# Performance work log

Hardware: AMD Instinct MI355X
Metric: run time of the kernel (lower is better)

## Reference

```python
import jax, jax.numpy as jnp
import numpy as np


def setup_inputs() -> dict:
    key = jax.random.key(0)
    kx, ke = jax.random.split(key)
    N, T, D, M = 64, 400, 1024, 256
    x = jax.random.normal(kx, (N, T, D), dtype=jnp.float32)
    embedding = jax.random.normal(ke, (M, D), dtype=jnp.float32)
    return {"x": x, "embedding": embedding}


def reference(x, embedding):
    # x: (N, T, D); embedding (codebook): (M, D)
    M, D = embedding.shape
    # L2_distance: normalize codebook rows, distances to detached x
    emb_norm = embedding / (jnp.linalg.norm(embedding, axis=1, keepdims=True) + 1e-4)
    x_flat = jax.lax.stop_gradient(x).reshape(-1, D)  # (N*T, D)
    distances = (jnp.sum(emb_norm ** 2, axis=1)[None, :]
                 + jnp.sum(x_flat ** 2, axis=1, keepdims=True)
                 - 2.0 * (x_flat @ emb_norm.T))  # (N*T, M)
    indices = jnp.argmin(distances, axis=-1)  # (N*T,)
    encodings = jax.nn.one_hot(indices, M, dtype=jnp.float32)  # (N*T, M)
    quantized = embedding[indices].reshape(x.shape)  # gather from UNnormalized codebook

    # commitment loss (both sides detached in original -> constant)
    commitment_loss = jnp.mean(
        (jax.lax.stop_gradient(x) - jax.lax.stop_gradient(quantized)) ** 2)

    # straight-through + average with quantized
    quantized_st = x + jax.lax.stop_gradient(quantized - x)
    quantized_ = (quantized_st + quantized) / 2.0

    avg_probs = jnp.mean(encodings, axis=0)  # (M,)
    perplexity = jnp.exp(-jnp.sum(avg_probs * jnp.log(avg_probs + 1e-10)))
    return quantized_, commitment_loss, perplexity
```

## Files before the change

kernel.cpp:

```cpp
#include <hip/hip_runtime.h>
#include <cstdint>
#include <cstddef>


typedef __attribute__((ext_vector_type(8))) short short8;
typedef __attribute__((ext_vector_type(4))) float f32x4;

namespace {
constexpr int kNT = 25600;
constexpr int kD  = 1024;
constexpr int kM  = 256;
constexpr size_t kQElems = (size_t)kNT * kD;

constexpr int WS_IMG_H = 0;
constexpr int WS_IMG_L = 131072;
constexpr int WS_E2N   = 262144;
constexpr int WS_SCL   = WS_E2N + kM;
constexpr int WS_E2R   = WS_SCL + kM;
constexpr int WS_COM   = WS_E2R + kM;
constexpr int WS_HIST  = WS_COM + 4;
constexpr int WS_ZERO_BYTES = (WS_HIST + kM - WS_COM) * 4;
}

typedef __attribute__((address_space(3))) unsigned int        lds_u32;
typedef const __attribute__((address_space(1))) unsigned int  glb_u32;
typedef const __attribute__((address_space(3))) char          lds_chc;

__device__ __forceinline__ void gl2lds16(const void* g, void* l) {
  __builtin_amdgcn_global_load_lds((glb_u32*)g, (lds_u32*)l, 16, 0, 0);
}

template <int OFF>
__device__ __forceinline__ short8 ldsr(lds_chc* p) {
  short8 r;
  asm volatile("ds_read_b128 %0, %1 offset:%c2" : "=v"(r) : "v"(p), "i"(OFF));
  return r;
}

__global__ __launch_bounds__(256) void vq_normalize(const float* __restrict__ emb,
                                                    float* __restrict__ ws) {
  const int m = blockIdx.x;
  const int t = threadIdx.x;
  const float4 v = reinterpret_cast<const float4*>(emb + (size_t)m * kD)[t];
  float s = v.x * v.x + v.y * v.y + v.z * v.z + v.w * v.w;
#pragma unroll
  for (int mask = 32; mask >= 1; mask >>= 1) s += __shfl_xor(s, mask);
  __shared__ float red[4];
  if ((t & 63) == 0) red[t >> 6] = s;
  __syncthreads();
  const float tot = red[0] + red[1] + red[2] + red[3];
  const float sc  = sqrtf(tot) + 1e-4f;
  const float inv = 1.0f / sc;
  const float4 nv = make_float4(v.x * inv, v.y * inv, v.z * inv, v.w * inv);

  float s2 = nv.x * nv.x + nv.y * nv.y + nv.z * nv.z + nv.w * nv.w;
#pragma unroll
  for (int mask = 32; mask >= 1; mask >>= 1) s2 += __shfl_xor(s2, mask);
  __syncthreads();
  if ((t & 63) == 0) red[t >> 6] = s2;
  __syncthreads();
  if (t == 0) {
    ws[WS_E2N + m] = red[0] + red[1] + red[2] + red[3];
    ws[WS_SCL + m] = sc;
    ws[WS_E2R + m] = tot;
  }

  unsigned short* imgh = (unsigned short*)(ws + WS_IMG_H);
  unsigned short* imgl = (unsigned short*)(ws + WS_IMG_L);
  const int c  = t >> 3;
  const int g  = (t >> 1) & 3;
  const int sq = g ^ ((m >> 1) & 3);
  const int base = c * 8192 + m * 32 + sq * 8 + 4 * (t & 1);
  ushort4 hq, lq;
#pragma unroll
  for (int j = 0; j < 4; ++j) {
    const float fv = (&nv.x)[j];
    const unsigned int b = __float_as_uint(fv);
    const unsigned short hi = (unsigned short)(b >> 16);
    const float lof = fv - __uint_as_float(b & 0xFFFF0000u);
    const unsigned short lo = (unsigned short)(__float_as_uint(lof) >> 16);
    (&hq.x)[j] = hi; (&lq.x)[j] = lo;
  }
  *(ushort4*)(imgh + base) = hq;
  *(ushort4*)(imgl + base) = lq;
}


#define RD8(BSEL, G, H0, H1, H2, H3, L0, L1, L2, L3)                           \
  H0 = ldsr<(BSEL) * 32768 + ((G) * 4 + 0) * 1024>(lbase);                     \
  H1 = ldsr<(BSEL) * 32768 + ((G) * 4 + 1) * 1024>(lbase);                     \
  H2 = ldsr<(BSEL) * 32768 + ((G) * 4 + 2) * 1024>(lbase);                     \
  H3 = ldsr<(BSEL) * 32768 + ((G) * 4 + 3) * 1024>(lbase);                     \
  L0 = ldsr<(BSEL) * 32768 + 16384 + ((G) * 4 + 0) * 1024>(lbase);             \
  L1 = ldsr<(BSEL) * 32768 + 16384 + ((G) * 4 + 1) * 1024>(lbase);             \
  L2 = ldsr<(BSEL) * 32768 + 16384 + ((G) * 4 + 2) * 1024>(lbase);             \
  L3 = ldsr<(BSEL) * 32768 + 16384 + ((G) * 4 + 3) * 1024>(lbase);

#define MM12(G, H0, H1, H2, H3, L0, L1, L2, L3)                                              \
  acc[(G) * 4 + 0] = __builtin_amdgcn_mfma_f32_16x16x32_bf16(ah, H0, acc[(G) * 4 + 0], 0, 0, 0); \
  acc[(G) * 4 + 1] = __builtin_amdgcn_mfma_f32_16x16x32_bf16(ah, H1, acc[(G) * 4 + 1], 0, 0, 0); \
  acc[(G) * 4 + 2] = __builtin_amdgcn_mfma_f32_16x16x32_bf16(ah, H2, acc[(G) * 4 + 2], 0, 0, 0); \
  acc[(G) * 4 + 3] = __builtin_amdgcn_mfma_f32_16x16x32_bf16(ah, H3, acc[(G) * 4 + 3], 0, 0, 0); \
  acc[(G) * 4 + 0] = __builtin_amdgcn_mfma_f32_16x16x32_bf16(ah, L0, acc[(G) * 4 + 0], 0, 0, 0); \
  acc[(G) * 4 + 1] = __builtin_amdgcn_mfma_f32_16x16x32_bf16(ah, L1, acc[(G) * 4 + 1], 0, 0, 0); \
  acc[(G) * 4 + 2] = __builtin_amdgcn_mfma_f32_16x16x32_bf16(ah, L2, acc[(G) * 4 + 2], 0, 0, 0); \
  acc[(G) * 4 + 3] = __builtin_amdgcn_mfma_f32_16x16x32_bf16(ah, L3, acc[(G) * 4 + 3], 0, 0, 0); \
  acc[(G) * 4 + 0] = __builtin_amdgcn_mfma_f32_16x16x32_bf16(al, H0, acc[(G) * 4 + 0], 0, 0, 0); \
  acc[(G) * 4 + 1] = __builtin_amdgcn_mfma_f32_16x16x32_bf16(al, H1, acc[(G) * 4 + 1], 0, 0, 0); \
  acc[(G) * 4 + 2] = __builtin_amdgcn_mfma_f32_16x16x32_bf16(al, H2, acc[(G) * 4 + 2], 0, 0, 0); \
  acc[(G) * 4 + 3] = __builtin_amdgcn_mfma_f32_16x16x32_bf16(al, H3, acc[(G) * 4 + 3], 0, 0, 0);

#define VQ_ITER(KC, BSEL, XC0, XC1, XN0, XN1)                                  \
  {                                                                            \
    const int kcn_ = ((KC) < 31) ? (KC) + 1 : 31;                              \
    const float* xp_ = xrow + kcn_ * 32;                                       \
    XN0 = *(const float4*)xp_;                                                 \
    XN1 = *(const float4*)(xp_ + 4);                                           \
    {                                                                          \
      const unsigned short* sg_ = simg + ((size_t)kcn_ << 13) + soff;          \
      char* dg_ = &buf[(BSEL) ^ 1][0] + ldst;                                  \
      _Pragma("unroll")                                                        \
      for (int it_ = 0; it_ < 8; ++it_)                                        \
        gl2lds16(sg_ + it_ * 512, dg_ + it_ * 1024);                           \
    }                                                                          \
    asm volatile("s_waitcnt vmcnt(10)" ::: "memory");                          \
    __builtin_amdgcn_s_barrier();                                              \
    asm volatile("" ::: "memory");                                             \
    short8 ha0_, ha1_, ha2_, ha3_, la0_, la1_, la2_, la3_;                     \
    short8 hb0_, hb1_, hb2_, hb3_, lb0_, lb1_, lb2_, lb3_;                     \
    RD8((BSEL), 0, ha0_, ha1_, ha2_, ha3_, la0_, la1_, la2_, la3_)             \
    RD8((BSEL), 1, hb0_, hb1_, hb2_, hb3_, lb0_, lb1_, lb2_, lb3_)             \
    short8 ah, al;                                                             \
    {                                                                          \
      union { short8 v; unsigned short u[8]; } H_, L_;                         \
      const float fx_[8] = {XC0.x, XC0.y, XC0.z, XC0.w,                        \
                            XC1.x, XC1.y, XC1.z, XC1.w};                       \
      _Pragma("unroll")                                                        \
      for (int jj_ = 0; jj_ < 8; ++jj_) {                                      \
        const float fv_ = fx_[jj_];                                            \
        const unsigned int b_ = __float_as_uint(fv_);                          \
        H_.u[jj_] = (unsigned short)(b_ >> 16);                                \
        const float lo_ = fv_ - __uint_as_float(b_ & 0xFFFF0000u);             \
        L_.u[jj_] = (unsigned short)(__float_as_uint(lo_) >> 16);              \
        x2 += fv_ * fv_;                                                       \
      }                                                                        \
      ah = H_.v; al = L_.v;                                                    \
    }                                                                          \
    asm volatile("s_waitcnt lgkmcnt(8)" ::: "memory");                         \
    __builtin_amdgcn_sched_barrier(0);                                         \
    MM12(0, ha0_, ha1_, ha2_, ha3_, la0_, la1_, la2_, la3_)                    \
    RD8((BSEL), 2, ha0_, ha1_, ha2_, ha3_, la0_, la1_, la2_, la3_)             \
    asm volatile("s_waitcnt lgkmcnt(8)" ::: "memory");                         \
    __builtin_amdgcn_sched_barrier(0);                                         \
    MM12(1, hb0_, hb1_, hb2_, hb3_, lb0_, lb1_, lb2_, lb3_)                    \
    RD8((BSEL), 3, hb0_, hb1_, hb2_, hb3_, lb0_, lb1_, lb2_, lb3_)             \
    asm volatile("s_waitcnt lgkmcnt(8)" ::: "memory");                         \
    __builtin_amdgcn_sched_barrier(0);                                         \
    MM12(2, ha0_, ha1_, ha2_, ha3_, la0_, la1_, la2_, la3_)                    \
    asm volatile("s_waitcnt lgkmcnt(0)" ::: "memory");                         \
    __builtin_amdgcn_sched_barrier(0);                                         \
    MM12(3, hb0_, hb1_, hb2_, hb3_, lb0_, lb1_, lb2_, lb3_)                    \
    asm volatile("" ::: "memory");                                             \
    __builtin_amdgcn_s_barrier();                                              \
    asm volatile("" ::: "memory");                                             \
  }

__global__ __launch_bounds__(256, 2) void vq_main(const float* __restrict__ x,
                                                  const float* __restrict__ emb,
                                                  const float* __restrict__ wsc,
                                                  float* __restrict__ out,
                                                  float* __restrict__ commit_sum,
                                                  int* __restrict__ hist) {
  __shared__ char buf[2][32768];

  const int t   = threadIdx.x;
  const int l   = t & 63;
  const int w   = t >> 6;
  const int r0  = blockIdx.x * 64 + w * 16;
  const int nlo = l & 15;
  const int q   = l >> 4;
  const int sq  = q ^ ((l >> 1) & 3);

  const unsigned short* imgH = (const unsigned short*)(wsc + WS_IMG_H);
  const unsigned short* imgL = (const unsigned short*)(wsc + WS_IMG_L);
  const unsigned short* simg = (w & 2) ? imgL : imgH;
  const int soff = (w & 1) * 4096 + l * 8;
  const int ldst = w * 8192;

  const float* xrow = x + (size_t)(r0 + nlo) * kD + q * 8;
  lds_chc* lbase = (lds_chc*)&buf[0][0] + nlo * 64 + sq * 16;

  f32x4 acc[16];
#pragma unroll
  for (int i = 0; i < 16; ++i) acc[i] = (f32x4)0.0f;
  float x2 = 0.0f;

  float4 xa0, xa1, xb0, xb1;
  xa0 = *(const float4*)xrow;
  xa1 = *(const float4*)(xrow + 4);
  {
    const unsigned short* sg = simg + soff;
    char* dg = &buf[0][0] + ldst;
#pragma unroll
    for (int it = 0; it < 8; ++it) gl2lds16(sg + it * 512, dg + it * 1024);
  }

#pragma unroll 1
  for (int kk = 0; kk < 32; kk += 2) {
    VQ_ITER(kk,     0, xa0, xa1, xb0, xb1)
    VQ_ITER(kk + 1, 1, xb0, xb1, xa0, xa1)
  }

  x2 += __shfl_xor(x2, 16);
  x2 += __shfl_xor(x2, 32);

  float bv[4] = {3.0e38f, 3.0e38f, 3.0e38f, 3.0e38f};
  int   bj[4] = {0, 0, 0, 0};
#pragma unroll
  for (int ct = 0; ct < 16; ++ct) {
    const int j = ct * 16 + nlo;
    const float e = wsc[WS_E2N + j];
#pragma unroll
    for (int rg = 0; rg < 4; ++rg) {
      const float v = e - 2.0f * acc[ct][rg];
      if (v < bv[rg] || (v == bv[rg] && j < bj[rg])) { bv[rg] = v; bj[rg] = j; }
    }
  }
#pragma unroll
  for (int mk = 1; mk <= 8; mk <<= 1) {
#pragma unroll
    for (int rg = 0; rg < 4; ++rg) {
      const float ov = __shfl_xor(bv[rg], mk);
      const int   oj = __shfl_xor(bj[rg], mk);
      if (ov < bv[rg] || (ov == bv[rg] && oj < bj[rg])) { bv[rg] = ov; bj[rg] = oj; }
    }
  }

  float clq = 0.0f;
#pragma unroll
  for (int rg = 0; rg < 4; ++rg) {
    const int j = bj[rg];
    const float xr2 = __shfl(x2, (q << 2) | rg);
    clq += xr2 + wsc[WS_E2R + j] - (wsc[WS_E2N + j] - bv[rg]) * wsc[WS_SCL + j];
  }
  if (nlo == 0) {
#pragma unroll
    for (int rg = 0; rg < 4; ++rg) atomicAdd(&hist[bj[rg]], 1);
  }
  float cs = (nlo == 0) ? clq : 0.0f;
  cs += __shfl_xor(cs, 16);
  cs += __shfl_xor(cs, 32);
  if (l == 0) atomicAdd(commit_sum, cs);

  const float4* emb4 = (const float4*)emb;
  float4* out4 = (float4*)out;
#pragma unroll
  for (int r = 0; r < 16; ++r) {
    const int j = __shfl(bj[r & 3], (r >> 2) << 4);
    const float4* s = emb4 + (size_t)j * (kD / 4);
    float4* d = out4 + (size_t)(r0 + r) * (kD / 4);
#pragma unroll
    for (int c = 0; c < 4; ++c) d[c * 64 + l] = s[c * 64 + l];
  }
}

__global__ __launch_bounds__(256) void vq_final(const int* __restrict__ hist,
                                                const float* __restrict__ commit_sum,
                                                float* __restrict__ out) {
  const int t = threadIdx.x;
  const float p = (float)hist[t] * (1.0f / (float)kNT);
  float s = p * logf(p + 1e-10f);
#pragma unroll
  for (int mask = 32; mask >= 1; mask >>= 1) s += __shfl_xor(s, mask);
  __shared__ float red[4];
  if ((t & 63) == 0) red[t >> 6] = s;
  __syncthreads();
  if (t == 0) {
    const float ent = red[0] + red[1] + red[2] + red[3];
    out[kQElems]     = commit_sum[0] * (1.0f / (float)kQElems);
    out[kQElems + 1] = expf(-ent);
  }
}

extern "C" void kernel_launch(void* const* d_in, const int* in_sizes, int n_in,
                              void* d_out, int out_size, void* d_ws, size_t ws_size,
                              hipStream_t stream) {
  (void)in_sizes; (void)n_in; (void)out_size; (void)ws_size;
  const float* x   = (const float*)d_in[0];
  const float* emb = (const float*)d_in[1];
  float* out = (float*)d_out;
  float* ws  = (float*)d_ws;

  hipMemsetAsync((char*)d_ws + (size_t)WS_COM * 4, 0, WS_ZERO_BYTES, stream);
  hipLaunchKernelGGL(vq_normalize, dim3(kM), dim3(256), 0, stream, emb, ws);
  hipLaunchKernelGGL(vq_main, dim3(kNT / 64), dim3(256), 0, stream,
                     x, emb, ws, out, ws + WS_COM, (int*)(ws + WS_HIST));
  hipLaunchKernelGGL(vq_final, dim3(1), dim3(256), 0, stream,
                     (const int*)(ws + WS_HIST), ws + WS_COM, out);
}
```

Baseline: 252.6 us.

## Repartition VQ GEMM so each wave owns a codebook slice with shared x tile

Restructures the main distance GEMM. Each wave now keeps its own 64-code slice of the bf16 hi/lo codebook in LDS, and the 64 rows of x are converted once and written into a shared LDS tile that all waves read as the A operand. Previously each wave held 16 rows and all 256 codes. The argmin is then done per wave and merged across waves through shared memory. The change also restages the pipeline (x loads two steps ahead, MFMA priority via setprio) and cuts LDS per block to 48KB. The aim is to reduce redundant codebook LDS reads and improve MFMA/DMA overlap, at the cost of a cross-wave reduction and extra barriers.

```diff
diff --git a/kernel.cpp b/kernel.cpp
--- a/kernel.cpp
+++ b/kernel.cpp
@@ -36,6 +36,15 @@
   asm volatile("ds_read_b128 %0, %1 offset:%c2" : "=v"(r) : "v"(p), "i"(OFF));
   return r;
 }
+template <int OFF>
+__device__ __forceinline__ void ldsw(lds_chc* p, short8 v) {
+  asm volatile("ds_write_b128 %0, %1 offset:%c2" :: "v"(p), "v"(v), "i"(OFF) : "memory");
+}
+__device__ __forceinline__ f32x4 gld4(const float* p) {
+  f32x4 r;
+  asm volatile("global_load_dwordx4 %0, %1, off" : "=v"(r) : "v"(p));
+  return r;
+}
 
 __global__ __launch_bounds__(256) void vq_normalize(const float* __restrict__ emb,
                                                     float* __restrict__ ws) {
@@ -86,83 +95,94 @@
 }
 
 
-#define RD8(BSEL, G, H0, H1, H2, H3, L0, L1, L2, L3)                           \
-  H0 = ldsr<(BSEL) * 32768 + ((G) * 4 + 0) * 1024>(lbase);                     \
-  H1 = ldsr<(BSEL) * 32768 + ((G) * 4 + 1) * 1024>(lbase);                     \
-  H2 = ldsr<(BSEL) * 32768 + ((G) * 4 + 2) * 1024>(lbase);                     \
-  H3 = ldsr<(BSEL) * 32768 + ((G) * 4 + 3) * 1024>(lbase);                     \
-  L0 = ldsr<(BSEL) * 32768 + 16384 + ((G) * 4 + 0) * 1024>(lbase);             \
-  L1 = ldsr<(BSEL) * 32768 + 16384 + ((G) * 4 + 1) * 1024>(lbase);             \
-  L2 = ldsr<(BSEL) * 32768 + 16384 + ((G) * 4 + 2) * 1024>(lbase);             \
-  L3 = ldsr<(BSEL) * 32768 + 16384 + ((G) * 4 + 3) * 1024>(lbase);
-
-#define MM12(G, H0, H1, H2, H3, L0, L1, L2, L3)                                              \
-  acc[(G) * 4 + 0] = __builtin_amdgcn_mfma_f32_16x16x32_bf16(ah, H0, acc[(G) * 4 + 0], 0, 0, 0); \
-  acc[(G) * 4 + 1] = __builtin_amdgcn_mfma_f32_16x16x32_bf16(ah, H1, acc[(G) * 4 + 1], 0, 0, 0); \
-  acc[(G) * 4 + 2] = __builtin_amdgcn_mfma_f32_16x16x32_bf16(ah, H2, acc[(G) * 4 + 2], 0, 0, 0); \
-  acc[(G) * 4 + 3] = __builtin_amdgcn_mfma_f32_16x16x32_bf16(ah, H3, acc[(G) * 4 + 3], 0, 0, 0); \
-  acc[(G) * 4 + 0] = __builtin_amdgcn_mfma_f32_16x16x32_bf16(ah, L0, acc[(G) * 4 + 0], 0, 0, 0); \
-  acc[(G) * 4 + 1] = __builtin_amdgcn_mfma_f32_16x16x32_bf16(ah, L1, acc[(G) * 4 + 1], 0, 0, 0); \
-  acc[(G) * 4 + 2] = __builtin_amdgcn_mfma_f32_16x16x32_bf16(ah, L2, acc[(G) * 4 + 2], 0, 0, 0); \
-  acc[(G) * 4 + 3] = __builtin_amdgcn_mfma_f32_16x16x32_bf16(ah, L3, acc[(G) * 4 + 3], 0, 0, 0); \
-  acc[(G) * 4 + 0] = __builtin_amdgcn_mfma_f32_16x16x32_bf16(al, H0, acc[(G) * 4 + 0], 0, 0, 0); \
-  acc[(G) * 4 + 1] = __builtin_amdgcn_mfma_f32_16x16x32_bf16(al, H1, acc[(G) * 4 + 1], 0, 0, 0); \
-  acc[(G) * 4 + 2] = __builtin_amdgcn_mfma_f32_16x16x32_bf16(al, H2, acc[(G) * 4 + 2], 0, 0, 0); \
-  acc[(G) * 4 + 3] = __builtin_amdgcn_mfma_f32_16x16x32_bf16(al, H3, acc[(G) * 4 + 3], 0, 0, 0);
-
-#define VQ_ITER(KC, BSEL, XC0, XC1, XN0, XN1)                                  \
+#define DMASTAGE(KCN)                                                          \
   {                                                                            \
-    const int kcn_ = ((KC) < 31) ? (KC) + 1 : 31;                              \
-    const float* xp_ = xrow + kcn_ * 32;                                       \
-    XN0 = *(const float4*)xp_;                                                 \
-    XN1 = *(const float4*)(xp_ + 4);                                           \
+    const unsigned short* gh_ = imgH + ((size_t)(KCN) << 13) + (w << 11) + (l << 3); \
+    const unsigned short* gl_ = imgL + ((size_t)(KCN) << 13) + (w << 11) + (l << 3); \
+    gl2lds16(gh_,        BslU);                                                \
+    gl2lds16(gh_ +  512, BslU + 1024);                                         \
+    gl2lds16(gh_ + 1024, BslU + 2048);                                         \
+    gl2lds16(gh_ + 1536, BslU + 3072);                                         \
+    gl2lds16(gl_,        BslU + 4096);                                         \
+    gl2lds16(gl_ +  512, BslU + 5120);                                         \
+    gl2lds16(gl_ + 1024, BslU + 6144);                                         \
+    gl2lds16(gl_ + 1536, BslU + 7168);                                         \
+  }
+
+#define CONV8(F0, F1, AH, AL)                                                  \
+  {                                                                            \
+    union { short8 v; unsigned short u[8]; } H_, L_;                           \
+    _Pragma("unroll")                                                          \
+    for (int jj_ = 0; jj_ < 8; ++jj_) {                                        \
+      const float fv_ = (jj_ < 4) ? (F0)[jj_] : (F1)[jj_ - 4];                 \
+      const unsigned int b_ = __float_as_uint(fv_);                            \
+      H_.u[jj_] = (unsigned short)(b_ >> 16);                                  \
+      const float lo_ = fv_ - __uint_as_float(b_ & 0xFFFF0000u);               \
+      L_.u[jj_] = (unsigned short)(__float_as_uint(lo_) >> 16);                \
+      x2 += fv_ * fv_;                                                         \
+    }                                                                          \
+    AH = H_.v; AL = L_.v;                                                      \
+  }
+
+#define MMQ(AR, B0, B1, B2, B3, RT)                                                        \
+  acc[RT][0] = __builtin_amdgcn_mfma_f32_16x16x32_bf16(AR, B0, acc[RT][0], 0, 0, 0);       \
+  acc[RT][1] = __builtin_amdgcn_mfma_f32_16x16x32_bf16(AR, B1, acc[RT][1], 0, 0, 0);       \
+  acc[RT][2] = __builtin_amdgcn_mfma_f32_16x16x32_bf16(AR, B2, acc[RT][2], 0, 0, 0);       \
+  acc[RT][3] = __builtin_amdgcn_mfma_f32_16x16x32_bf16(AR, B3, acc[RT][3], 0, 0, 0);
+#define MMPASS(A0, A1, A2, A3, B0, B1, B2, B3)                                 \
+  MMQ(A0, B0, B1, B2, B3, 0) MMQ(A1, B0, B1, B2, B3, 1)                        \
+  MMQ(A2, B0, B1, B2, B3, 2) MMQ(A3, B0, B1, B2, B3, 3)
+
+#define VQ_ITER5(KC, XB, XC0, XC1, XN0, XN1)                                   \
+  {                                                                            \
+    asm volatile("s_waitcnt vmcnt(2)" ::: "memory");          \
+    __builtin_amdgcn_sched_barrier(0);                                         \
+    short8 a0h, a1h, a2h, a3h, a0l, a1l, a2l, a3l;                             \
+    short8 b0h, b1h, b2h, b3h, b0l, b1l, b2l, b3l;                             \
+    a0h = ldsr<32768 + (XB) * 8192 + 0 * 1024>(pA);                            \
+    a1h = ldsr<32768 + (XB) * 8192 + 1 * 1024>(pA);                            \
+    a2h = ldsr<32768 + (XB) * 8192 + 2 * 1024>(pA);                            \
+    a3h = ldsr<32768 + (XB) * 8192 + 3 * 1024>(pA);                            \
+    a0l = ldsr<32768 + (XB) * 8192 + 4096 + 0 * 1024>(pA);                     \
+    a1l = ldsr<32768 + (XB) * 8192 + 4096 + 1 * 1024>(pA);                     \
+    a2l = ldsr<32768 + (XB) * 8192 + 4096 + 2 * 1024>(pA);                     \
+    a3l = ldsr<32768 + (XB) * 8192 + 4096 + 3 * 1024>(pA);                     \
+    b0h = ldsr<0 * 1024>(pB);                                                  \
+    b1h = ldsr<1 * 1024>(pB);                                                  \
+    b2h = ldsr<2 * 1024>(pB);                                                  \
+    b3h = ldsr<3 * 1024>(pB);                                                  \
+    b0l = ldsr<4096 + 0 * 1024>(pB);                                           \
+    b1l = ldsr<4096 + 1 * 1024>(pB);                                           \
+    b2l = ldsr<4096 + 2 * 1024>(pB);                                           \
+    b3l = ldsr<4096 + 3 * 1024>(pB);                                           \
+    asm volatile("s_waitcnt lgkmcnt(0)" ::: "memory");      \
+    __builtin_amdgcn_sched_barrier(0);                                         \
+    {                      \
+      const int kcn_ = ((KC) + 1 < 32) ? (KC) + 1 : 31;                        \
+      DMASTAGE(kcn_)                                                           \
+    }                                                                          \
     {                                                                          \
-      const unsigned short* sg_ = simg + ((size_t)kcn_ << 13) + soff;          \
-      char* dg_ = &buf[(BSEL) ^ 1][0] + ldst;                                  \
-      _Pragma("unroll")                                                        \
-      for (int it_ = 0; it_ < 8; ++it_)                                        \
-        gl2lds16(sg_ + it_ * 512, dg_ + it_ * 1024);                           \
+      const int kc2_ = ((KC) + 2 < 32) ? (KC) + 2 : 31;                        \
+      XN0 = gld4(xrow + kc2_ * 32);                                            \
+      XN1 = gld4(xrow + kc2_ * 32 + 4);                                        \
     }                                                                          \
-    asm volatile("s_waitcnt vmcnt(10)" ::: "memory");                          \
+    __builtin_amdgcn_s_setprio(1);                                             \
+    MMPASS(a0h, a1h, a2h, a3h, b0h, b1h, b2h, b3h)                  \
+    MMPASS(a0h, a1h, a2h, a3h, b0l, b1l, b2l, b3l)                  \
+    __builtin_amdgcn_s_setprio(0);                                             \
+    asm volatile("s_waitcnt vmcnt(10)" ::: "memory");       \
+    __builtin_amdgcn_sched_barrier(0);                                         \
+    if ((KC) < 31) {                                                           \
+      short8 cah, cal;                                                         \
+      CONV8(XC0, XC1, cah, cal)                                                \
+      ldsw<32768 + ((XB) ^ 1) * 8192 + 0>(pW, cah);                            \
+      ldsw<32768 + ((XB) ^ 1) * 8192 + 4096>(pW, cal);                         \
+    }                                                                          \
+    __builtin_amdgcn_s_setprio(1);                                             \
+    MMPASS(a0l, a1l, a2l, a3l, b0h, b1h, b2h, b3h)                  \
+    __builtin_amdgcn_s_setprio(0);                                             \
+    asm volatile("s_waitcnt lgkmcnt(0)" ::: "memory");      \
     __builtin_amdgcn_s_barrier();                                              \
-    asm volatile("" ::: "memory");                                             \
-    short8 ha0_, ha1_, ha2_, ha3_, la0_, la1_, la2_, la3_;                     \
-    short8 hb0_, hb1_, hb2_, hb3_, lb0_, lb1_, lb2_, lb3_;                     \
-    RD8((BSEL), 0, ha0_, ha1_, ha2_, ha3_, la0_, la1_, la2_, la3_)             \
-    RD8((BSEL), 1, hb0_, hb1_, hb2_, hb3_, lb0_, lb1_, lb2_, lb3_)             \
-    short8 ah, al;                                                             \
-    {                                                                          \
-      union { short8 v; unsigned short u[8]; } H_, L_;                         \
-      const float fx_[8] = {XC0.x, XC0.y, XC0.z, XC0.w,                        \
-                            XC1.x, XC1.y, XC1.z, XC1.w};                       \
-      _Pragma("unroll")                                                        \
-      for (int jj_ = 0; jj_ < 8; ++jj_) {                                      \
-        const float fv_ = fx_[jj_];                                            \
-        const unsigned int b_ = __float_as_uint(fv_);                          \
-        H_.u[jj_] = (unsigned short)(b_ >> 16);                                \
-        const float lo_ = fv_ - __uint_as_float(b_ & 0xFFFF0000u);             \
-        L_.u[jj_] = (unsigned short)(__float_as_uint(lo_) >> 16);              \
-        x2 += fv_ * fv_;                                                       \
-      }                                                                        \
-      ah = H_.v; al = L_.v;                                                    \
-    }                                                                          \
-    asm volatile("s_waitcnt lgkmcnt(8)" ::: "memory");                         \
-    __builtin_amdgcn_sched_barrier(0);                                         \
-    MM12(0, ha0_, ha1_, ha2_, ha3_, la0_, la1_, la2_, la3_)                    \
-    RD8((BSEL), 2, ha0_, ha1_, ha2_, ha3_, la0_, la1_, la2_, la3_)             \
-    asm volatile("s_waitcnt lgkmcnt(8)" ::: "memory");                         \
-    __builtin_amdgcn_sched_barrier(0);                                         \
-    MM12(1, hb0_, hb1_, hb2_, hb3_, lb0_, lb1_, lb2_, lb3_)                    \
-    RD8((BSEL), 3, hb0_, hb1_, hb2_, hb3_, lb0_, lb1_, lb2_, lb3_)             \
-    asm volatile("s_waitcnt lgkmcnt(8)" ::: "memory");                         \
-    __builtin_amdgcn_sched_barrier(0);                                         \
-    MM12(2, ha0_, ha1_, ha2_, ha3_, la0_, la1_, la2_, la3_)                    \
-    asm volatile("s_waitcnt lgkmcnt(0)" ::: "memory");                         \
-    __builtin_amdgcn_sched_barrier(0);                                         \
-    MM12(3, hb0_, hb1_, hb2_, hb3_, lb0_, lb1_, lb2_, lb3_)                    \
-    asm volatile("" ::: "memory");                                             \
-    __builtin_amdgcn_s_barrier();                                              \
-    asm volatile("" ::: "memory");                                             \
   }
 
 __global__ __launch_bounds__(256, 2) void vq_main(const float* __restrict__ x,
@@ -171,94 +191,138 @@
                                                   float* __restrict__ out,
                                                   float* __restrict__ commit_sum,
                                                   int* __restrict__ hist) {
-  __shared__ char buf[2][32768];
+  __shared__ char pool[49152];
+  __shared__ float x2s[64];
+  __shared__ float bvp[4][64];
+  __shared__ int   bjp[4][64];
+  __shared__ int   idx_s[64];
 
   const int t   = threadIdx.x;
   const int l   = t & 63;
   const int w   = t >> 6;
-  const int r0  = blockIdx.x * 64 + w * 16;
   const int nlo = l & 15;
-  const int q   = l >> 4;
-  const int sq  = q ^ ((l >> 1) & 3);
+  const int kq  = l >> 4;
+  const int blk0 = blockIdx.x * 64;
 
   const unsigned short* imgH = (const unsigned short*)(wsc + WS_IMG_H);
   const unsigned short* imgL = (const unsigned short*)(wsc + WS_IMG_L);
-  const unsigned short* simg = (w & 2) ? imgL : imgH;
-  const int soff = (w & 1) * 4096 + l * 8;
-  const int ldst = w * 8192;
-
-  const float* xrow = x + (size_t)(r0 + nlo) * kD + q * 8;
-  lds_chc* lbase = (lds_chc*)&buf[0][0] + nlo * 64 + sq * 16;
-
-  f32x4 acc[16];
-#pragma unroll
-  for (int i = 0; i < 16; ++i) acc[i] = (f32x4)0.0f;
+  char* BslU = pool + w * 8192;
+
+  const float* xrow = x + (size_t)(blk0 + w * 16 + nlo) * kD + kq * 8;
+
+  const int sqz = kq ^ ((nlo >> 1) & 3);
+  lds_chc* base = (lds_chc*)pool;
+  lds_chc* pA = base + nlo * 64 + sqz * 16;
+  lds_chc* pB = base + w * 8192 + nlo * 64 + sqz * 16;
+  lds_chc* pW = pA + w * 1024;
+
+  f32x4 acc[4][4];
+#pragma unroll
+  for (int i = 0; i < 4; ++i)
+#pragma unroll
+    for (int j = 0; j < 4; ++j) acc[i][j] = (f32x4)0.0f;
   float x2 = 0.0f;
 
-  float4 xa0, xa1, xb0, xb1;
-  xa0 = *(const float4*)xrow;
-  xa1 = *(const float4*)(xrow + 4);
+  f32x4 xa0 = gld4(xrow);
+  f32x4 xa1 = gld4(xrow + 4);
+  DMASTAGE(0)
+  f32x4 xb0 = gld4(xrow + 32);
+  f32x4 xb1 = gld4(xrow + 36);
+  asm volatile("s_waitcnt vmcnt(10)" ::: "memory");
+  __builtin_amdgcn_sched_barrier(0);
   {
-    const unsigned short* sg = simg + soff;
-    char* dg = &buf[0][0] + ldst;
-#pragma unroll
-    for (int it = 0; it < 8; ++it) gl2lds16(sg + it * 512, dg + it * 1024);
-  }
+    short8 cah, cal;
+    CONV8(xa0, xa1, cah, cal)
+    ldsw<32768 + 0>(pW, cah);
+    ldsw<32768 + 4096>(pW, cal);
+  }
+  asm volatile("s_waitcnt lgkmcnt(0)" ::: "memory");
+  __builtin_amdgcn_s_barrier();
 
 #pragma unroll 1
   for (int kk = 0; kk < 32; kk += 2) {
-    VQ_ITER(kk,     0, xa0, xa1, xb0, xb1)
-    VQ_ITER(kk + 1, 1, xb0, xb1, xa0, xa1)
-  }
+    VQ_ITER5(kk,     0, xb0, xb1, xa0, xa1)
+    VQ_ITER5(kk + 1, 1, xa0, xa1, xb0, xb1)
+  }
+
+  asm volatile("s_waitcnt vmcnt(0)"
+               :: "v"(xa0), "v"(xa1), "v"(xb0), "v"(xb1) : "memory");
 
   x2 += __shfl_xor(x2, 16);
   x2 += __shfl_xor(x2, 32);
-
-  float bv[4] = {3.0e38f, 3.0e38f, 3.0e38f, 3.0e38f};
-  int   bj[4] = {0, 0, 0, 0};
-#pragma unroll
-  for (int ct = 0; ct < 16; ++ct) {
-    const int j = ct * 16 + nlo;
-    const float e = wsc[WS_E2N + j];
-#pragma unroll
-    for (int rg = 0; rg < 4; ++rg) {
-      const float v = e - 2.0f * acc[ct][rg];
-      if (v < bv[rg] || (v == bv[rg] && j < bj[rg])) { bv[rg] = v; bj[rg] = j; }
+  if (l < 16) x2s[w * 16 + l] = x2;
+
+  float eN[4];
+#pragma unroll
+  for (int ct = 0; ct < 4; ++ct) eN[ct] = wsc[WS_E2N + w * 64 + ct * 16 + nlo];
+
+  float bv[4][4]; int bj[4][4];
+#pragma unroll
+  for (int rt = 0; rt < 4; ++rt)
+#pragma unroll
+    for (int rg = 0; rg < 4; ++rg) { bv[rt][rg] = 3.0e38f; bj[rt][rg] = 0; }
+#pragma unroll
+  for (int ct = 0; ct < 4; ++ct) {
+    const int j = w * 64 + ct * 16 + nlo;
+#pragma unroll
+    for (int rt = 0; rt < 4; ++rt)
+#pragma unroll
+      for (int rg = 0; rg < 4; ++rg) {
+        const float v = eN[ct] - 2.0f * acc[rt][ct][rg];
+        if (v < bv[rt][rg] || (v == bv[rt][rg] && j < bj[rt][rg])) {
+          bv[rt][rg] = v; bj[rt][rg] = j;
+        }
+      }
+  }
+#pragma unroll
+  for (int mk = 1; mk <= 8; mk <<= 1) {
+#pragma unroll
+    for (int rt = 0; rt < 4; ++rt)
+#pragma unroll
+      for (int rg = 0; rg < 4; ++rg) {
+        const float ov = __shfl_xor(bv[rt][rg], mk);
+        const int   oj = __shfl_xor(bj[rt][rg], mk);
+        if (ov < bv[rt][rg] || (ov == bv[rt][rg] && oj < bj[rt][rg])) {
+          bv[rt][rg] = ov; bj[rt][rg] = oj;
+        }
+      }
+  }
+  if (nlo == 0) {
+#pragma unroll
+    for (int rt = 0; rt < 4; ++rt)
+#pragma unroll
+      for (int rg = 0; rg < 4; ++rg) {
+        const int row = rt * 16 + kq * 4 + rg;
+        bvp[w][row] = bv[rt][rg];
+        bjp[w][row] = bj[rt][rg];
+      }
+  }
+  __syncthreads();
+
+  if (t < 64) {
+    const int row = t;
+    float v = bvp[0][row]; int j = bjp[0][row];
+#pragma unroll
+    for (int wv = 1; wv < 4; ++wv) {
+      const float v2 = bvp[wv][row]; const int j2 = bjp[wv][row];
+      if (v2 < v || (v2 == v && j2 < j)) { v = v2; j = j2; }
     }
-  }
-#pragma unroll
-  for (int mk = 1; mk <= 8; mk <<= 1) {
-#pragma unroll
-    for (int rg = 0; rg < 4; ++rg) {
-      const float ov = __shfl_xor(bv[rg], mk);
-      const int   oj = __shfl_xor(bj[rg], mk);
-      if (ov < bv[rg] || (ov == bv[rg] && oj < bj[rg])) { bv[rg] = ov; bj[rg] = oj; }
-    }
-  }
-
-  float clq = 0.0f;
-#pragma unroll
-  for (int rg = 0; rg < 4; ++rg) {
-    const int j = bj[rg];
-    const float xr2 = __shfl(x2, (q << 2) | rg);
-    clq += xr2 + wsc[WS_E2R + j] - (wsc[WS_E2N + j] - bv[rg]) * wsc[WS_SCL + j];
-  }
-  if (nlo == 0) {
-#pragma unroll
-    for (int rg = 0; rg < 4; ++rg) atomicAdd(&hist[bj[rg]], 1);
-  }
-  float cs = (nlo == 0) ? clq : 0.0f;
-  cs += __shfl_xor(cs, 16);
-  cs += __shfl_xor(cs, 32);
-  if (l == 0) atomicAdd(commit_sum, cs);
+    idx_s[row] = j;
+    atomicAdd(&hist[j], 1);
+    float cl = x2s[row] + wsc[WS_E2R + j] - (wsc[WS_E2N + j] - v) * wsc[WS_SCL + j];
+#pragma unroll
+    for (int mk = 1; mk <= 32; mk <<= 1) cl += __shfl_xor(cl, mk);
+    if (t == 0) atomicAdd(commit_sum, cl);
+  }
+  __syncthreads();
 
   const float4* emb4 = (const float4*)emb;
   float4* out4 = (float4*)out;
-#pragma unroll
-  for (int r = 0; r < 16; ++r) {
-    const int j = __shfl(bj[r & 3], (r >> 2) << 4);
+#pragma unroll 2
+  for (int rr = 0; rr < 16; ++rr) {
+    const int j = idx_s[w * 16 + rr];
     const float4* s = emb4 + (size_t)j * (kD / 4);
-    float4* d = out4 + (size_t)(r0 + r) * (kD / 4);
+    float4* d = out4 + (size_t)(blk0 + w * 16 + rr) * (kD / 4);
 #pragma unroll
     for (int c = 0; c < 4; ++c) d[c * 64 + l] = s[c * 64 + l];
   }
```

Result: faster. 228.3 us (-9.6%).
